# Kernel optimization log

Hardware: AMD Instinct MI355X
Metric: run time of the kernel (lower is better)

Reference implementation:

```python
import jax, jax.numpy as jnp
import numpy as np

B, C, H, W = 16, 192, 64, 64
L = 256           # number of quantization levels (len(sos.unique_values))
EXTREMA = 10.0    # codebook support roughly [-extrema, extrema]


def setup_inputs() -> dict:
    key = jax.random.key(0)
    k1, k2, k3 = jax.random.split(key, 3)
    inputs = jax.random.normal(k1, (B, C, H, W), dtype=jnp.float32) * 3.0
    means = jax.random.normal(k2, (B, C, H, W), dtype=jnp.float32)
    # sorted codebook of unique quantizer output values (sos.unique_values)
    raw = jax.random.uniform(k3, (L,), dtype=jnp.float32,
                             minval=-EXTREMA, maxval=EXTREMA)
    unique_values = jnp.sort(raw)
    return {"inputs": inputs, "means": means, "unique_values": unique_values}


def _nearest_symbols(v, unique_values):
    # Parallel binary search over the sorted codebook; equivalent to the
    # original per-element argmin(|keys - x|) in transform_map.
    L_ = unique_values.shape[0]
    idx = jnp.searchsorted(unique_values, v)          # in [0, L]
    idx = jnp.clip(idx, 1, L_ - 1)
    left = unique_values[idx - 1]
    right = unique_values[idx]
    # on ties, argmin picks the lower index -> use <=
    return jnp.where(jnp.abs(v - left) <= jnp.abs(v - right), idx - 1, idx)


def reference(inputs, means, unique_values):
    # quantize(mode='symbols'): subtract means, snap to nearest codebook
    # value, map value -> integer symbol via the sorted codebook.
    v = inputs - means
    symbols = _nearest_symbols(v, unique_values)      # int32 [B,C,H,W]
    # dequantize: symbol -> float codebook value (map_cdf_sos), add means.
    dequant = unique_values[symbols] + means          # float32 [B,C,H,W]
    return dequant, symbols
```

## Files before the change

kernel.cpp:

```cpp
#include <hip/hip_runtime.h>


#define LVL 256

__global__ __launch_bounds__(256) void agc_quant_kernel(
    const float* __restrict__ inputs,
    const float* __restrict__ means,
    const float* __restrict__ uv,
    float* __restrict__ out_deq,
    float* __restrict__ out_sym,
    int n4, int n)
{
    __shared__ float s_uv[LVL];
    s_uv[threadIdx.x] = uv[threadIdx.x];
    __syncthreads();

    int i = blockIdx.x * blockDim.x + threadIdx.x;
    if (i < n4) {
        float4 in = reinterpret_cast<const float4*>(inputs)[i];
        float4 mn = reinterpret_cast<const float4*>(means)[i];

        float vs[4] = {in.x - mn.x, in.y - mn.y, in.z - mn.z, in.w - mn.w};
        float ms[4] = {mn.x, mn.y, mn.z, mn.w};
        float dq[4], sy[4];

        #pragma unroll
        for (int k = 0; k < 4; ++k) {
            float v = vs[k];
            int lo = 0, hi = LVL;
            #pragma unroll
            for (int s = 0; s < 8; ++s) {
                int mid = (lo + hi) >> 1;
                bool go_right = (s_uv[mid] < v);
                lo = go_right ? (mid + 1) : lo;
                hi = go_right ? hi : mid;
            }
            int idx = min(max(lo, 1), LVL - 1);
            float left  = s_uv[idx - 1];
            float right = s_uv[idx];
            bool take_left = (fabsf(v - left) <= fabsf(v - right));
            int   sym = take_left ? (idx - 1) : idx;
            float val = take_left ? left : right;
            dq[k] = val + ms[k];
            sy[k] = (float)sym;
        }

        reinterpret_cast<float4*>(out_deq)[i] = make_float4(dq[0], dq[1], dq[2], dq[3]);
        reinterpret_cast<float4*>(out_sym)[i] = make_float4(sy[0], sy[1], sy[2], sy[3]);
    }

    if (blockIdx.x == 0 && threadIdx.x == 0) {
        for (int j = n4 * 4; j < n; ++j) {
            float m = means[j];
            float v = inputs[j] - m;
            int lo = 0, hi = LVL;
            for (int s = 0; s < 8; ++s) {
                int mid = (lo + hi) >> 1;
                bool go_right = (s_uv[mid] < v);
                lo = go_right ? (mid + 1) : lo;
                hi = go_right ? hi : mid;
            }
            int idx = min(max(lo, 1), LVL - 1);
            float left  = s_uv[idx - 1];
            float right = s_uv[idx];
            bool take_left = (fabsf(v - left) <= fabsf(v - right));
            int   sym = take_left ? (idx - 1) : idx;
            float val = take_left ? left : right;
            out_deq[j] = val + m;
            out_sym[j] = (float)sym;
        }
    }
}

extern "C" void kernel_launch(void* const* d_in, const int* in_sizes, int n_in,
                              void* d_out, int out_size, void* d_ws, size_t ws_size,
                              hipStream_t stream) {
    const float* inputs = (const float*)d_in[0];
    const float* means  = (const float*)d_in[1];
    const float* uv     = (const float*)d_in[2];

    int n  = in_sizes[0];
    int n4 = n / 4;

    float* out     = (float*)d_out;
    float* out_deq = out;
    float* out_sym = out + n;

    int threads = 256;
    int blocks  = (n4 + threads - 1) / threads;
    agc_quant_kernel<<<blocks, threads, 0, stream>>>(
        inputs, means, uv, out_deq, out_sym, n4, n);
}
```

Before: 180.1 us.

## Replace per-element binary search with uniform-bucket lookup table

Adds a prep kernel that splits the codebook range into 2048 uniform buckets. Each bucket stores its bracketing codebook pair, or a fallback start index when the bucket spans a codebook boundary. The main kernel loads this table into shared memory, computes the bucket index arithmetically, and runs a short linear scan only in ambiguous buckets. This replaces the 8-step dependent shared-memory binary search, and the main kernel becomes grid-stride with at most 2048 blocks. In exchange it adds an extra kernel launch, a per-block 24KB shared-memory table load, and divergent linear scans for values near boundaries.

After: 184.9 us. 2.7% more time.

```diff
diff --git a/kernel.cpp b/kernel.cpp
--- a/kernel.cpp
+++ b/kernel.cpp
@@ -2,8 +2,154 @@
 
 
 #define LVL 256
-
-__global__ __launch_bounds__(256) void agc_quant_kernel(
+#define NB  2048
+#define MAINBLOCKS 2048
+
+__global__ __launch_bounds__(256) void agc_build_lut(
+    const float* __restrict__ uv, float* __restrict__ ws)
+{
+    __shared__ float s_uv[LVL];
+    if (threadIdx.x < LVL) s_uv[threadIdx.x] = uv[threadIdx.x];
+    __syncthreads();
+
+    int b = blockIdx.x * blockDim.x + threadIdx.x;
+    if (b >= NB) return;
+
+    float lo    = s_uv[0];
+    float width = (s_uv[LVL - 1] - lo) / (float)NB;
+
+    float eL = (b == 0)      ? -__builtin_inff() : lo + (float)(b - 1) * width;
+    float eU = (b == NB - 1) ?  __builtin_inff() : lo + (float)(b + 2) * width;
+
+    int A, Bc;
+    {
+        int l = 0, h = LVL;
+        #pragma unroll
+        for (int s = 0; s < 8; ++s) {
+            int m = (l + h) >> 1;
+            bool r = (s_uv[m] < eL);
+            l = r ? (m + 1) : l;
+            h = r ? h : m;
+        }
+        A = l;
+        l = 0; h = LVL;
+        #pragma unroll
+        for (int s = 0; s < 8; ++s) {
+            int m = (l + h) >> 1;
+            bool r = (s_uv[m] < eU);
+            l = r ? (m + 1) : l;
+            h = r ? h : m;
+        }
+        Bc = l;
+    }
+    int cA = min(max(A, 1), LVL - 1);
+    int cB = min(max(Bc, 1), LVL - 1);
+
+    float* lutL = ws;
+    float* lutR = ws + NB;
+    int*   lutS = reinterpret_cast<int*>(ws + 2 * NB);
+
+    if (cA == cB) {
+        lutL[b] = s_uv[cA - 1];
+        lutR[b] = s_uv[cA];
+        lutS[b] = cA - 1;
+    } else {
+        lutL[b] = 0.0f;
+        lutR[b] = 0.0f;
+        lutS[b] = -(A + 1);
+    }
+}
+
+__global__ __launch_bounds__(256) void agc_quant_lut(
+    const float* __restrict__ inputs,
+    const float* __restrict__ means,
+    const float* __restrict__ uv,
+    const float* __restrict__ ws,
+    float* __restrict__ out_deq,
+    float* __restrict__ out_sym,
+    int n4, int n, int stride)
+{
+    __shared__ float s_uv[LVL];
+    __shared__ float s_L[NB];
+    __shared__ float s_R[NB];
+    __shared__ int   s_S[NB];
+
+    s_uv[threadIdx.x] = uv[threadIdx.x];
+    {
+        const float4* wL = reinterpret_cast<const float4*>(ws);
+        const float4* wR = reinterpret_cast<const float4*>(ws + NB);
+        const int4*   wS = reinterpret_cast<const int4*>(ws + 2 * NB);
+        #pragma unroll
+        for (int t = 0; t < NB / 4 / 256; ++t) {
+            int j = t * 256 + threadIdx.x;
+            reinterpret_cast<float4*>(s_L)[j] = wL[j];
+            reinterpret_cast<float4*>(s_R)[j] = wR[j];
+            reinterpret_cast<int4*>(s_S)[j]   = wS[j];
+        }
+    }
+    __syncthreads();
+
+    const float lo    = s_uv[0];
+    const float scale = (float)NB / (s_uv[LVL - 1] - lo);
+
+    for (int i = blockIdx.x * blockDim.x + threadIdx.x; i < n4; i += stride) {
+        float4 in = reinterpret_cast<const float4*>(inputs)[i];
+        float4 mn = reinterpret_cast<const float4*>(means)[i];
+
+        float vs[4] = {in.x - mn.x, in.y - mn.y, in.z - mn.z, in.w - mn.w};
+        float ms[4] = {mn.x, mn.y, mn.z, mn.w};
+        float dq[4], sy[4];
+
+        #pragma unroll
+        for (int k = 0; k < 4; ++k) {
+            float v = vs[k];
+            int b = (int)floorf((v - lo) * scale);
+            b = min(max(b, 0), NB - 1);
+
+            float left  = s_L[b];
+            float right = s_R[b];
+            int   code  = s_S[b];
+            int   base  = code;
+
+            if (code < 0) {
+                int s = -code - 1;
+                while (s < LVL && s_uv[s] < v) ++s;
+                int idx = min(max(s, 1), LVL - 1);
+                left  = s_uv[idx - 1];
+                right = s_uv[idx];
+                base  = idx - 1;
+            }
+
+            bool tl = (fabsf(v - left) <= fabsf(v - right));
+            sy[k] = (float)(tl ? base : base + 1);
+            dq[k] = (tl ? left : right) + ms[k];
+        }
+
+        reinterpret_cast<float4*>(out_deq)[i] = make_float4(dq[0], dq[1], dq[2], dq[3]);
+        reinterpret_cast<float4*>(out_sym)[i] = make_float4(sy[0], sy[1], sy[2], sy[3]);
+    }
+
+    if (blockIdx.x == 0 && threadIdx.x == 0) {
+        for (int j = n4 * 4; j < n; ++j) {
+            float m = means[j];
+            float v = inputs[j] - m;
+            int l = 0, h = LVL;
+            for (int s = 0; s < 8; ++s) {
+                int mm = (l + h) >> 1;
+                bool r = (s_uv[mm] < v);
+                l = r ? (mm + 1) : l;
+                h = r ? h : mm;
+            }
+            int idx = min(max(l, 1), LVL - 1);
+            float left = s_uv[idx - 1], right = s_uv[idx];
+            bool tl = fabsf(v - left) <= fabsf(v - right);
+            out_deq[j] = (tl ? left : right) + m;
+            out_sym[j] = (float)(tl ? idx - 1 : idx);
+        }
+    }
+}
+
+__global__ __launch_bounds__(256) void agc_quant_fallback(
     const float* __restrict__ inputs,
     const float* __restrict__ means,
     const float* __restrict__ uv,
@@ -19,11 +165,9 @@
     if (i < n4) {
         float4 in = reinterpret_cast<const float4*>(inputs)[i];
         float4 mn = reinterpret_cast<const float4*>(means)[i];
-
         float vs[4] = {in.x - mn.x, in.y - mn.y, in.z - mn.z, in.w - mn.w};
         float ms[4] = {mn.x, mn.y, mn.z, mn.w};
         float dq[4], sy[4];
-
         #pragma unroll
         for (int k = 0; k < 4; ++k) {
             float v = vs[k];
@@ -31,24 +175,19 @@
             #pragma unroll
             for (int s = 0; s < 8; ++s) {
                 int mid = (lo + hi) >> 1;
-                bool go_right = (s_uv[mid] < v);
-                lo = go_right ? (mid + 1) : lo;
-                hi = go_right ? hi : mid;
+                bool r = (s_uv[mid] < v);
+                lo = r ? (mid + 1) : lo;
+                hi = r ? hi : mid;
             }
             int idx = min(max(lo, 1), LVL - 1);
-            float left  = s_uv[idx - 1];
-            float right = s_uv[idx];
-            bool take_left = (fabsf(v - left) <= fabsf(v - right));
-            int   sym = take_left ? (idx - 1) : idx;
-            float val = take_left ? left : right;
-            dq[k] = val + ms[k];
-            sy[k] = (float)sym;
-        }
-
+            float left = s_uv[idx - 1], right = s_uv[idx];
+            bool tl = (fabsf(v - left) <= fabsf(v - right));
+            sy[k] = (float)(tl ? idx - 1 : idx);
+            dq[k] = (tl ? left : right) + ms[k];
+        }
         reinterpret_cast<float4*>(out_deq)[i] = make_float4(dq[0], dq[1], dq[2], dq[3]);
         reinterpret_cast<float4*>(out_sym)[i] = make_float4(sy[0], sy[1], sy[2], sy[3]);
     }
-
     if (blockIdx.x == 0 && threadIdx.x == 0) {
         for (int j = n4 * 4; j < n; ++j) {
             float m = means[j];
@@ -56,25 +195,23 @@
             int lo = 0, hi = LVL;
             for (int s = 0; s < 8; ++s) {
                 int mid = (lo + hi) >> 1;
-                bool go_right = (s_uv[mid] < v);
-                lo = go_right ? (mid + 1) : lo;
-                hi = go_right ? hi : mid;
+                bool r = (s_uv[mid] < v);
+                lo = r ? (mid + 1) : lo;
+                hi = r ? hi : mid;
             }
             int idx = min(max(lo, 1), LVL - 1);
-            float left  = s_uv[idx - 1];
-            float right = s_uv[idx];
-            bool take_left = (fabsf(v - left) <= fabsf(v - right));
-            int   sym = take_left ? (idx - 1) : idx;
-            float val = take_left ? left : right;
-            out_deq[j] = val + m;
-            out_sym[j] = (float)sym;
+            float left = s_uv[idx - 1], right = s_uv[idx];
+            bool tl = fabsf(v - left) <= fabsf(v - right);
+            out_deq[j] = (tl ? left : right) + m;
+            out_sym[j] = (float)(tl ? idx - 1 : idx);
         }
     }
 }
 
 extern "C" void kernel_launch(void* const* d_in, const int* in_sizes, int n_in,
                               void* d_out, int out_size, void* d_ws, size_t ws_size,
-                              hipStream_t stream) {
+                              hipStream_t stream)
+{
     const float* inputs = (const float*)d_in[0];
     const float* means  = (const float*)d_in[1];
     const float* uv     = (const float*)d_in[2];
@@ -86,8 +223,20 @@
     float* out_deq = out;
     float* out_sym = out + n;
 
-    int threads = 256;
-    int blocks  = (n4 + threads - 1) / threads;
-    agc_quant_kernel<<<blocks, threads, 0, stream>>>(
-        inputs, means, uv, out_deq, out_sym, n4, n);
-}
+    size_t need = (size_t)NB * 3 * sizeof(float);
+    if (d_ws != nullptr && ws_size >= need) {
+        agc_build_lut<<<NB / 256, 256, 0, stream>>>(uv, (float*)d_ws);
+
+        int blocks = (n4 + 255) / 256;
+        if (blocks > MAINBLOCKS) blocks = MAINBLOCKS;
+        if (blocks < 1)          blocks = 1;
+        agc_quant_lut<<<blocks, 256, 0, stream>>>(
+            inputs, means, uv, (const float*)d_ws,
+            out_deq, out_sym, n4, n, blocks * 256);
+    } else {
+        int blocks = (n4 + 255) / 256;
+        if (blocks < 1) blocks = 1;
+        agc_quant_fallback<<<blocks, 256, 0, stream>>>(
+            inputs, means, uv, out_deq, out_sym, n4, n);
+    }
+}
```
